# Kernel optimization log

Measured on AMD Instinct MI355X. Metric: run time of the kernel, lower is better.

The kernel has to match this reference:

```python
import jax, jax.numpy as jnp
import numpy as np
from jax import lax

DT = 0.1


def setup_inputs() -> dict:
    key = jax.random.key(0)
    k1, k2, k3, k4 = jax.random.split(key, 4)
    Bsz, L, D, N, O = 32, 2048, 256, 64, 256
    x = jax.random.normal(k1, (Bsz, L, D), dtype=jnp.float32)
    # Shift A by 3*I so Re(eig(A)) > 0 -> bilinear-discretized A_tilde is stable
    A = jax.random.uniform(k2, (N, N), dtype=jnp.float32) + 3.0 * jnp.eye(N, dtype=jnp.float32)
    B = jax.random.uniform(k3, (N, D), dtype=jnp.float32)
    C = jax.random.uniform(k4, (O, N), dtype=jnp.float32)
    return {"x": x, "A": A, "B": B, "C": C}


def _s4_forward(x, A, B, C):
    N = A.shape[0]
    I = jnp.eye(N, dtype=A.dtype)
    # Bilinear discretization (as written in the torch source)
    tmp_inv = jnp.linalg.inv(I + A * (DT / 2))
    A_tilde = tmp_inv @ (I - A * (DT / 2))          # [N, N]
    B_tilde = (tmp_inv @ B) * DT                    # [N, D]

    L = x.shape[1]

    # K[i] = C @ A_tilde^i @ B_tilde; carry M = A_tilde^i @ B_tilde
    def step(M, _):
        return A_tilde @ M, C @ M                    # emit [O, D]

    _, K = lax.scan(step, B_tilde, None, length=L)   # K: [L, O, D]

    n = 2 * L - 1  # length after torch's F.pad(x, (0,0,0,L-1))
    x_fft = jnp.fft.rfft(x, n=n, axis=1)             # [B, F, D] complex
    K_fft = jnp.fft.rfft(K, n=n, axis=0)             # [F, O, D] complex
    y_fft = jnp.einsum('bfi,foi->bfo', x_fft, K_fft)
    y = jnp.fft.irfft(y_fft, n=n, axis=1)[:, :L]     # [B, L, O]
    return y


def reference(x, A, B, C):
    return _s4_forward(x, A, B, C)
```

## Files before the change

kernel.cpp:

```cpp
#include <hip/hip_runtime.h>

#define B_SZ   32
#define LEN    2048
#define DIM    256
#define NST    64
#define OUTD   256
#define CHUNK  64
#define NCHUNK (LEN / CHUNK)
#define ROWS   (B_SZ * LEN)

#define OFF_AT   0
#define OFF_A64  4096
#define OFF_MT   8192
#define OFF_S    12288
#define OFF_INST 77824
#define OFF_U    143360
#define OFF_H    4337664
#define OFF_V    OFF_H
#define WS_FLOATS (OFF_H + ROWS * 64)

__global__ __launch_bounds__(256) void k_fused0(const float* __restrict__ A,
                                                const float* __restrict__ Bm,
                                                const float* __restrict__ x,
                                                float* __restrict__ ws) {
  __shared__ __align__(16) float sh[9088];
  const int t = threadIdx.x;

  if (blockIdx.x == 0) {
    float* Pa  = sh;
    float* Pb  = sh + 4352;
    float* rbM = sh + 8704;
    float* rbI = sh + 8832;
    float* cb  = sh + 8960;

    const int tc = t & 63;
    const int tr = t >> 6;
    float M[16], Iv[16];
    for (int i = 0; i < 16; ++i) {
      int r = 16 * tr + i;
      M[i] = 0.05f * A[r * 64 + tc] + (r == tc ? 1.0f : 0.0f);
      Iv[i] = (r == tc) ? 1.0f : 0.0f;
    }
    if (tr == 0) { rbM[tc] = M[0]; rbI[tc] = Iv[0]; }
    if (tc == 0)
      for (int i = 0; i < 16; ++i) cb[16 * tr + i] = M[i];
    __syncthreads();

#pragma unroll
    for (int k = 0; k < 64; ++k) {
      const int cur = (k & 1) * 64, nxt = ((k + 1) & 1) * 64;
      float rinv = 1.0f / rbM[cur + k];
      float rM = rbM[cur + tc] * rinv;
      float rI = rbI[cur + tc] * rinv;
#pragma unroll
      for (int i = 0; i < 16; ++i) {
        int r = 16 * tr + i;
        if (r == k) { M[i] = rM; Iv[i] = rI; }
        else {
          float f = cb[cur + r];
          M[i] = fmaf(-f, rM, M[i]);
          Iv[i] = fmaf(-f, rI, Iv[i]);
        }
      }
      if (k < 63) {
        if (tr == ((k + 1) >> 4)) {
          rbM[nxt + tc] = M[(k + 1) & 15];
          rbI[nxt + tc] = Iv[(k + 1) & 15];
        }
        if (tc == k + 1)
          for (int i = 0; i < 16; ++i) cb[nxt + 16 * tr + i] = M[i];
      }
      __syncthreads();
    }

    for (int i = 0; i < 16; ++i) {
      int r = 16 * tr + i;
      ws[OFF_AT + r * 64 + tc] = 2.0f * Iv[i] - (r == tc ? 1.0f : 0.0f);
      Pa[r * 65 + tc] = Iv[i];
    }
    __syncthreads();
    for (int i = 0; i < 16; ++i) {
      int m = 16 * tr + i;
      ws[OFF_MT + m * 64 + tc] = Pa[tc * 65 + m];
    }
    __syncthreads();

    for (int i = 0; i < 16; ++i) {
      int r = 16 * tr + i;
      Pa[r * 68 + tc] = 2.0f * Iv[i] - (r == tc ? 1.0f : 0.0f);
    }
    __syncthreads();
    float* src = Pa; float* dst = Pb;
    const int r0 = 4 * (t >> 4), c0 = 4 * (t & 15);
    for (int it = 0; it < 6; ++it) {
      float acc[4][4] = {};
      for (int k = 0; k < 64; ++k) {
        float4 bv = *(const float4*)(src + k * 68 + c0);
        for (int i = 0; i < 4; ++i) {
          float av = src[(r0 + i) * 68 + k];
          acc[i][0] = fmaf(av, bv.x, acc[i][0]);
          acc[i][1] = fmaf(av, bv.y, acc[i][1]);
          acc[i][2] = fmaf(av, bv.z, acc[i][2]);
          acc[i][3] = fmaf(av, bv.w, acc[i][3]);
        }
      }
      for (int i = 0; i < 4; ++i)
        *(float4*)(dst + (r0 + i) * 68 + c0) =
            make_float4(acc[i][0], acc[i][1], acc[i][2], acc[i][3]);
      __syncthreads();
      float* tmp = src; src = dst; dst = tmp;
    }
    for (int i = 0; i < 4; ++i) {
      int f = 4 * (t + 256 * i);
      int r = f >> 6, c = f & 63;
      *(float4*)(ws + OFF_A64 + f) = *(const float4*)(src + r * 68 + c);
    }
  } else {
    float* xsT = sh;
    float* bsT = sh + 4352;
    const int rowbase = (blockIdx.x - 1) * 64;
    const int r0 = 4 * (t >> 4), m0 = 4 * (t & 15);
    float acc[4][4] = {};
    for (int db = 0; db < 4; ++db) {
      int d0 = db * 64;
      for (int i = 0; i < 4; ++i) {
        int e = 4 * (t + 256 * i);
        int rr = e >> 6, dd = e & 63;
        float4 xv = *(const float4*)(x + (size_t)(rowbase + rr) * 256 + d0 + dd);
        xsT[(dd + 0) * 68 + rr] = xv.x;
        xsT[(dd + 1) * 68 + rr] = xv.y;
        xsT[(dd + 2) * 68 + rr] = xv.z;
        xsT[(dd + 3) * 68 + rr] = xv.w;
        float4 bv = *(const float4*)(Bm + (size_t)rr * 256 + d0 + dd);
        bsT[(dd + 0) * 68 + rr] = bv.x;
        bsT[(dd + 1) * 68 + rr] = bv.y;
        bsT[(dd + 2) * 68 + rr] = bv.z;
        bsT[(dd + 3) * 68 + rr] = bv.w;
      }
      __syncthreads();
      for (int k = 0; k < 64; ++k) {
        float4 av4 = *(const float4*)(xsT + k * 68 + r0);
        float4 bv4 = *(const float4*)(bsT + k * 68 + m0);
        float av[4] = {av4.x, av4.y, av4.z, av4.w};
        float bv[4] = {bv4.x, bv4.y, bv4.z, bv4.w};
        for (int i = 0; i < 4; ++i)
          for (int j = 0; j < 4; ++j) acc[i][j] = fmaf(av[i], bv[j], acc[i][j]);
      }
      __syncthreads();
    }
    float* v = ws + OFF_V;
    for (int i = 0; i < 4; ++i)
      *(float4*)(v + (size_t)(rowbase + r0 + i) * 64 + m0) =
          make_float4(acc[i][0], acc[i][1], acc[i][2], acc[i][3]);
  }
}

__global__ __launch_bounds__(256) void k_umm(float* __restrict__ ws) {
  __shared__ __align__(16) float vT[64 * 68];
  __shared__ __align__(16) float mts[64 * 68];
  const int t = threadIdx.x;
  const int rowbase = blockIdx.x * 64;
  const float* v = ws + OFF_V;
  for (int i = 0; i < 4; ++i) {
    int e = 4 * (t + 256 * i);
    int rr = e >> 6, mm = e & 63;
    *(float4*)(mts + rr * 68 + mm) = *(const float4*)(ws + OFF_MT + e);
    float4 vv = *(const float4*)(v + (size_t)(rowbase + rr) * 64 + mm);
    vT[(mm + 0) * 68 + rr] = vv.x;
    vT[(mm + 1) * 68 + rr] = vv.y;
    vT[(mm + 2) * 68 + rr] = vv.z;
    vT[(mm + 3) * 68 + rr] = vv.w;
  }
  __syncthreads();
  const int r0 = 4 * (t >> 4), n0 = 4 * (t & 15);
  float acc[4][4] = {};
  for (int k = 0; k < 64; ++k) {
    float4 av4 = *(const float4*)(vT + k * 68 + r0);
    float4 bv4 = *(const float4*)(mts + k * 68 + n0);
    float av[4] = {av4.x, av4.y, av4.z, av4.w};
    float bv[4] = {bv4.x, bv4.y, bv4.z, bv4.w};
    for (int i = 0; i < 4; ++i)
      for (int j = 0; j < 4; ++j) acc[i][j] = fmaf(av[i], bv[j], acc[i][j]);
  }
  float* u = ws + OFF_U;
  for (int i = 0; i < 4; ++i)
    *(float4*)(u + (size_t)(rowbase + r0 + i) * 64 + n0) =
        make_float4(0.1f * acc[i][0], 0.1f * acc[i][1], 0.1f * acc[i][2],
                    0.1f * acc[i][3]);
}

__device__ __forceinline__ void load_areg(const float* __restrict__ M, int r,
                                          int q, float areg[16]) {
  const float4* ap = (const float4*)(M + r * 64 + q * 16);
  float4 a0 = ap[0], a1 = ap[1], a2 = ap[2], a3 = ap[3];
  areg[0] = a0.x; areg[1] = a0.y; areg[2] = a0.z; areg[3] = a0.w;
  areg[4] = a1.x; areg[5] = a1.y; areg[6] = a1.z; areg[7] = a1.w;
  areg[8] = a2.x; areg[9] = a2.y; areg[10] = a2.z; areg[11] = a2.w;
  areg[12] = a3.x; areg[13] = a3.y; areg[14] = a3.z; areg[15] = a3.w;
}

__device__ __forceinline__ float matvec_step(const float areg[16],
                                             const float* __restrict__ hcur,
                                             float* __restrict__ part, int r,
                                             int q, int t) {
  float4 ha = *(const float4*)(hcur + q * 16);
  float4 hb = *(const float4*)(hcur + q * 16 + 4);
  float4 hc = *(const float4*)(hcur + q * 16 + 8);
  float4 hd = *(const float4*)(hcur + q * 16 + 12);
  float p0 = fmaf(areg[0], ha.x, fmaf(areg[4], hb.x, fmaf(areg[8], hc.x, areg[12] * hd.x)));
  float p1 = fmaf(areg[1], ha.y, fmaf(areg[5], hb.y, fmaf(areg[9], hc.y, areg[13] * hd.y)));
  float p2 = fmaf(areg[2], ha.z, fmaf(areg[6], hb.z, fmaf(areg[10], hc.z, areg[14] * hd.z)));
  float p3 = fmaf(areg[3], ha.w, fmaf(areg[7], hb.w, fmaf(areg[11], hc.w, areg[15] * hd.w)));
  part[q * 68 + r] = (p0 + p1) + (p2 + p3);
  __syncthreads();
  float s = 0.0f;
  if (t < 64) s = part[t] + part[68 + t] + part[136 + t] + part[204 + t];
  return s;
}

__global__ __launch_bounds__(256) void k_chunk(float* __restrict__ ws, int phase) {
  __shared__ __align__(16) float hcur[64];
  __shared__ __align__(16) float part[4 * 68];
  __shared__ __align__(16) float ulds[CHUNK * 64];
  const int t = threadIdx.x;
  const int c = blockIdx.x, b = blockIdx.y;
  const int r = t & 63, q = t >> 6;
  float areg[16];
  load_areg(ws + OFF_AT, r, q, areg);
  const float* u = ws + OFF_U + (size_t)(b * LEN + c * CHUNK) * 64;
  for (int i = 0; i < 4; ++i) {
    int e = 4 * (t + 256 * i);
    *(float4*)(ulds + e) = *(const float4*)(u + e);
  }
  if (t < 64)
    hcur[t] = (phase == 3) ? ws[OFF_INST + (b * NCHUNK + c) * 64 + t] : 0.0f;
  __syncthreads();
  for (int st = 0; st < CHUNK; ++st) {
    float s = matvec_step(areg, hcur, part, r, q, t);
    if (t < 64) {
      float hn = s + ulds[st * 64 + t];
      hcur[t] = hn;
      if (phase == 3)
        ws[OFF_H + (size_t)(b * LEN + c * CHUNK + st) * 64 + t] = hn;
      else if (st == CHUNK - 1)
        ws[OFF_S + (b * NCHUNK + c) * 64 + t] = hn;
    }
    __syncthreads();
  }
}

__global__ __launch_bounds__(256) void k_carry(float* __restrict__ ws) {
  __shared__ __align__(16) float hcur[64];
  __shared__ __align__(16) float part[4 * 68];
  __shared__ __align__(16) float slds[NCHUNK * 64];
  const int t = threadIdx.x;
  const int b = blockIdx.x;
  const int r = t & 63, q = t >> 6;
  float areg[16];
  load_areg(ws + OFF_A64, r, q, areg);
  for (int i = 0; i < 2; ++i) {
    int e = 4 * (t + 256 * i);
    *(float4*)(slds + e) = *(const float4*)(ws + OFF_S + b * NCHUNK * 64 + e);
  }
  if (t < 64) {
    hcur[t] = 0.0f;
    ws[OFF_INST + (b * NCHUNK) * 64 + t] = 0.0f;
  }
  __syncthreads();
  for (int c = 1; c < NCHUNK; ++c) {
    float s = matvec_step(areg, hcur, part, r, q, t);
    if (t < 64) {
      float hn = s + slds[(c - 1) * 64 + t];
      hcur[t] = hn;
      ws[OFF_INST + (b * NCHUNK + c) * 64 + t] = hn;
    }
    __syncthreads();
  }
}

__global__ __launch_bounds__(256) void k_ygemm(const float* __restrict__ Cm,
                                               const float* __restrict__ ws,
                                               float* __restrict__ y) {
  __shared__ __align__(16) float hs[64 * 68];
  __shared__ __align__(16) float cs[64 * 68];
  const int t = threadIdx.x;
  const int rowbase = blockIdx.x * 64;
  const int o0 = blockIdx.y * 64;
  const float* h = ws + OFF_H;
  for (int i = 0; i < 4; ++i) {
    int e = 4 * (t + 256 * i);
    int rr = e >> 6, nn = e & 63;
    *(float4*)(hs + rr * 68 + nn) =
        *(const float4*)(h + (size_t)rowbase * 64 + e);
    float4 cv = *(const float4*)(Cm + (size_t)(o0 + rr) * 64 + nn);
    cs[(nn + 0) * 68 + rr] = cv.x;
    cs[(nn + 1) * 68 + rr] = cv.y;
    cs[(nn + 2) * 68 + rr] = cv.z;
    cs[(nn + 3) * 68 + rr] = cv.w;
  }
  __syncthreads();
  const int tr = t >> 4, tc = t & 15;
  const int r0 = tr * 4, c0 = tc * 4;
  float acc[4][4] = {};
  for (int k = 0; k < 64; ++k) {
    float4 cv4 = *(const float4*)(cs + k * 68 + c0);
    float cv[4] = {cv4.x, cv4.y, cv4.z, cv4.w};
    for (int i = 0; i < 4; ++i) {
      float hv = hs[(r0 + i) * 68 + k];
      for (int j = 0; j < 4; ++j) acc[i][j] = fmaf(hv, cv[j], acc[i][j]);
    }
  }
  for (int i = 0; i < 4; ++i)
    *(float4*)(y + (size_t)(rowbase + r0 + i) * 256 + o0 + c0) =
        make_float4(acc[i][0], acc[i][1], acc[i][2], acc[i][3]);
}

extern "C" void kernel_launch(void* const* d_in, const int* in_sizes, int n_in,
                              void* d_out, int out_size, void* d_ws,
                              size_t ws_size, hipStream_t stream) {
  const float* x = (const float*)d_in[0];
  const float* A = (const float*)d_in[1];
  const float* Bm = (const float*)d_in[2];
  const float* Cm = (const float*)d_in[3];
  float* y = (float*)d_out;
  float* ws = (float*)d_ws;
  if (ws_size < (size_t)WS_FLOATS * sizeof(float)) return;

  hipLaunchKernelGGL(k_fused0, dim3(1 + ROWS / 64), dim3(256), 0, stream, A, Bm,
                     x, ws);
  hipLaunchKernelGGL(k_umm, dim3(ROWS / 64), dim3(256), 0, stream, ws);
  hipLaunchKernelGGL(k_chunk, dim3(NCHUNK, B_SZ), dim3(256), 0, stream, ws, 1);
  hipLaunchKernelGGL(k_carry, dim3(B_SZ), dim3(256), 0, stream, ws);
  hipLaunchKernelGGL(k_chunk, dim3(NCHUNK, B_SZ), dim3(256), 0, stream, ws, 3);
  hipLaunchKernelGGL(k_ygemm, dim3(ROWS / 64, OUTD / 64), dim3(256), 0, stream,
                     Cm, ws, y);
}
```

Before: 258.8 us.

## Fold input matrix into output projection, drop k_umm, retile GEMMs with async LDS loads

Stops transforming the x·B product by the inverse matrix in a separate k_umm pass. Instead the scan runs on the untransformed state v, and the inverse (times DT) is folded into a precomputed C' = 0.1·C·Inv used by the output GEMM. This removes one full-size GEMM pass and its global-memory round trip. The x·B and y GEMMs are retiled to 128-row tiles with 8x4 and 8x8 register blocking, XOR-swizzled LDS, double buffering and global_load_lds direct loads, which raises register pressure and lowers occupancy.

```diff
diff --git a/kernel.cpp b/kernel.cpp
--- a/kernel.cpp
+++ b/kernel.cpp
@@ -11,27 +11,61 @@
 
 #define OFF_AT   0
 #define OFF_A64  4096
-#define OFF_MT   8192
-#define OFF_S    12288
-#define OFF_INST 77824
-#define OFF_U    143360
-#define OFF_H    4337664
-#define OFF_V    OFF_H
-#define WS_FLOATS (OFF_H + ROWS * 64)
+#define OFF_CP   8192
+#define OFF_S    24576
+#define OFF_INST 90112
+#define OFF_V    155648
+#define OFF_H    OFF_V
+#define WS_FLOATS (OFF_V + (size_t)ROWS * 64)
+
+__device__ __forceinline__ void gload16(const float* gp, float* lds_base,
+                                        int lane_off_f) {
+#if __has_builtin(__builtin_amdgcn_global_load_lds)
+  (void)lane_off_f;
+  __builtin_amdgcn_global_load_lds(
+      (const __attribute__((address_space(1))) unsigned int*)gp,
+      (__attribute__((address_space(3))) unsigned int*)lds_base, 16, 0, 0);
+#else
+  float4 tmp = *(const float4*)gp;
+  *(float4*)(lds_base + lane_off_f) = tmp;
+#endif
+}
+
+__device__ __forceinline__ void mm64(float* dst, const float* a, const float* b,
+                                     int t) {
+  const int r0 = 4 * (t >> 4), c0 = 4 * (t & 15);
+  float acc[4][4] = {};
+  for (int k = 0; k < 64; ++k) {
+    float4 bv = *(const float4*)(b + k * 68 + c0);
+    for (int i = 0; i < 4; ++i) {
+      float av = a[(r0 + i) * 68 + k];
+      acc[i][0] = fmaf(av, bv.x, acc[i][0]);
+      acc[i][1] = fmaf(av, bv.y, acc[i][1]);
+      acc[i][2] = fmaf(av, bv.z, acc[i][2]);
+      acc[i][3] = fmaf(av, bv.w, acc[i][3]);
+    }
+  }
+  for (int i = 0; i < 4; ++i)
+    *(float4*)(dst + (r0 + i) * 68 + c0) =
+        make_float4(acc[i][0], acc[i][1], acc[i][2], acc[i][3]);
+  __syncthreads();
+}
 
 __global__ __launch_bounds__(256) void k_fused0(const float* __restrict__ A,
                                                 const float* __restrict__ Bm,
+                                                const float* __restrict__ Cm,
                                                 const float* __restrict__ x,
                                                 float* __restrict__ ws) {
-  __shared__ __align__(16) float sh[9088];
+  __shared__ __align__(16) float sh[13056];
   const int t = threadIdx.x;
 
   if (blockIdx.x == 0) {
-    float* Pa  = sh;
-    float* Pb  = sh + 4352;
-    float* rbM = sh + 8704;
-    float* rbI = sh + 8832;
-    float* cb  = sh + 8960;
+    float* Pa = sh;
+    float* Pb = sh + 4352;
+    float* Pc = sh + 8704;
+    float* rbM = Pc;
+    float* rbI = Pc + 128;
+    float* cb  = Pc + 256;
 
     const int tc = t & 63;
     const int tr = t >> 6;
@@ -75,118 +109,120 @@
 
     for (int i = 0; i < 16; ++i) {
       int r = 16 * tr + i;
-      ws[OFF_AT + r * 64 + tc] = 2.0f * Iv[i] - (r == tc ? 1.0f : 0.0f);
-      Pa[r * 65 + tc] = Iv[i];
-    }
-    __syncthreads();
-    for (int i = 0; i < 16; ++i) {
-      int m = 16 * tr + i;
-      ws[OFF_MT + m * 64 + tc] = Pa[tc * 65 + m];
-    }
-    __syncthreads();
-
+      float at = 2.0f * Iv[i] - (r == tc ? 1.0f : 0.0f);
+      ws[OFF_AT + r * 64 + tc] = at;
+      Pa[r * 68 + tc] = at;
+      Pc[r * 68 + tc] = Iv[i];
+    }
+    __syncthreads();
+
+    mm64(Pb, Pa, Pa, t);
+    mm64(Pa, Pb, Pb, t);
+    mm64(Pb, Pa, Pa, t);
+    mm64(Pa, Pb, Pb, t);
+    mm64(Pb, Pa, Pa, t);
+    mm64(Pa, Pb, Pb, t);
     for (int i = 0; i < 16; ++i) {
       int r = 16 * tr + i;
-      Pa[r * 68 + tc] = 2.0f * Iv[i] - (r == tc ? 1.0f : 0.0f);
-    }
-    __syncthreads();
-    float* src = Pa; float* dst = Pb;
-    const int r0 = 4 * (t >> 4), c0 = 4 * (t & 15);
-    for (int it = 0; it < 6; ++it) {
-      float acc[4][4] = {};
-      for (int k = 0; k < 64; ++k) {
-        float4 bv = *(const float4*)(src + k * 68 + c0);
-        for (int i = 0; i < 4; ++i) {
-          float av = src[(r0 + i) * 68 + k];
-          acc[i][0] = fmaf(av, bv.x, acc[i][0]);
-          acc[i][1] = fmaf(av, bv.y, acc[i][1]);
-          acc[i][2] = fmaf(av, bv.z, acc[i][2]);
-          acc[i][3] = fmaf(av, bv.w, acc[i][3]);
+      ws[OFF_A64 + r * 64 + tc] = Pa[r * 68 + tc];
+    }
+
+    {
+      const float* Crow = Cm + (size_t)t * 64;
+      float4 acc4[16];
+      for (int q = 0; q < 16; ++q) acc4[q] = make_float4(0.f, 0.f, 0.f, 0.f);
+      for (int k = 0; k < 64; k += 4) {
+        float4 c4 = *(const float4*)(Crow + k);
+        float ck[4] = {c4.x, c4.y, c4.z, c4.w};
+#pragma unroll
+        for (int kk = 0; kk < 4; ++kk) {
+          const float* mrow = Pc + (k + kk) * 68;
+          float c = ck[kk];
+#pragma unroll
+          for (int q = 0; q < 16; ++q) {
+            float4 mv = *(const float4*)(mrow + 4 * q);
+            acc4[q].x = fmaf(c, mv.x, acc4[q].x);
+            acc4[q].y = fmaf(c, mv.y, acc4[q].y);
+            acc4[q].z = fmaf(c, mv.z, acc4[q].z);
+            acc4[q].w = fmaf(c, mv.w, acc4[q].w);
+          }
         }
       }
-      for (int i = 0; i < 4; ++i)
-        *(float4*)(dst + (r0 + i) * 68 + c0) =
-            make_float4(acc[i][0], acc[i][1], acc[i][2], acc[i][3]);
+      float* cp = ws + OFF_CP + (size_t)t * 64;
+      for (int q = 0; q < 16; ++q)
+        *(float4*)(cp + 4 * q) =
+            make_float4(0.1f * acc4[q].x, 0.1f * acc4[q].y, 0.1f * acc4[q].z,
+                        0.1f * acc4[q].w);
+    }
+  } else {
+    float* xs0 = sh;
+    float* xs1 = sh + 4096;
+    float* bs0 = sh + 8192;
+    float* bs1 = sh + 10240;
+    const int w = t >> 6, lane = t & 63;
+    const int ro8 = lane >> 3, kq8 = lane & 7;
+    const int rowbase = ((int)blockIdx.x - 1) * 128;
+
+    auto stage = [&](int d0, float* xbuf, float* bbuf) {
+#pragma unroll
+      for (int c = 0; c < 4; ++c) {
+        int q = 4 * w + c;
+        const float* gp = x + (size_t)(rowbase + 8 * q + ro8) * 256 + d0 +
+                          4 * (kq8 ^ (q & 7));
+        gload16(gp, xbuf + q * 256, lane * 4);
+      }
+#pragma unroll
+      for (int c = 0; c < 2; ++c) {
+        int q = 2 * w + c;
+        const float* gp =
+            Bm + (size_t)(8 * q + ro8) * 256 + d0 + 4 * (kq8 ^ q);
+        gload16(gp, bbuf + q * 256, lane * 4);
+      }
+    };
+
+    stage(0, xs0, bs0);
+    const int g = lane >> 4, lm = lane & 15;
+    const int r0 = 32 * w + 8 * g, m0 = 4 * lm;
+    const int ka = 4 * ((4 * w + g) & 7);
+    const int kb = 4 * ((lm >> 1) & 7);
+    float acc[8][4] = {};
+    float* xc = xs0; float* xn = xs1; float* bc = bs0; float* bn = bs1;
+    __syncthreads();
+
+    for (int s = 0; s < 8; ++s) {
+      if (s < 7) stage((s + 1) * 32, xn, bn);
+      const float* xa = xc + r0 * 32;
+      const float* bb = bc + m0 * 32;
+#pragma unroll
+      for (int k0 = 0; k0 < 32; k0 += 4) {
+        float4 a4[8], b4[4];
+#pragma unroll
+        for (int i = 0; i < 8; ++i)
+          a4[i] = *(const float4*)(xa + i * 32 + (k0 ^ ka));
+#pragma unroll
+        for (int j = 0; j < 4; ++j)
+          b4[j] = *(const float4*)(bb + j * 32 + (k0 ^ kb));
+#pragma unroll
+        for (int i = 0; i < 8; ++i)
+#pragma unroll
+          for (int j = 0; j < 4; ++j) {
+            acc[i][j] = fmaf(a4[i].x, b4[j].x, acc[i][j]);
+            acc[i][j] = fmaf(a4[i].y, b4[j].y, acc[i][j]);
+            acc[i][j] = fmaf(a4[i].z, b4[j].z, acc[i][j]);
+            acc[i][j] = fmaf(a4[i].w, b4[j].w, acc[i][j]);
+          }
+      }
       __syncthreads();
-      float* tmp = src; src = dst; dst = tmp;
-    }
-    for (int i = 0; i < 4; ++i) {
-      int f = 4 * (t + 256 * i);
-      int r = f >> 6, c = f & 63;
-      *(float4*)(ws + OFF_A64 + f) = *(const float4*)(src + r * 68 + c);
-    }
-  } else {
-    float* xsT = sh;
-    float* bsT = sh + 4352;
-    const int rowbase = (blockIdx.x - 1) * 64;
-    const int r0 = 4 * (t >> 4), m0 = 4 * (t & 15);
-    float acc[4][4] = {};
-    for (int db = 0; db < 4; ++db) {
-      int d0 = db * 64;
-      for (int i = 0; i < 4; ++i) {
-        int e = 4 * (t + 256 * i);
-        int rr = e >> 6, dd = e & 63;
-        float4 xv = *(const float4*)(x + (size_t)(rowbase + rr) * 256 + d0 + dd);
-        xsT[(dd + 0) * 68 + rr] = xv.x;
-        xsT[(dd + 1) * 68 + rr] = xv.y;
-        xsT[(dd + 2) * 68 + rr] = xv.z;
-        xsT[(dd + 3) * 68 + rr] = xv.w;
-        float4 bv = *(const float4*)(Bm + (size_t)rr * 256 + d0 + dd);
-        bsT[(dd + 0) * 68 + rr] = bv.x;
-        bsT[(dd + 1) * 68 + rr] = bv.y;
-        bsT[(dd + 2) * 68 + rr] = bv.z;
-        bsT[(dd + 3) * 68 + rr] = bv.w;
-      }
-      __syncthreads();
-      for (int k = 0; k < 64; ++k) {
-        float4 av4 = *(const float4*)(xsT + k * 68 + r0);
-        float4 bv4 = *(const float4*)(bsT + k * 68 + m0);
-        float av[4] = {av4.x, av4.y, av4.z, av4.w};
-        float bv[4] = {bv4.x, bv4.y, bv4.z, bv4.w};
-        for (int i = 0; i < 4; ++i)
-          for (int j = 0; j < 4; ++j) acc[i][j] = fmaf(av[i], bv[j], acc[i][j]);
-      }
-      __syncthreads();
+      float* tp;
+      tp = xc; xc = xn; xn = tp;
+      tp = bc; bc = bn; bn = tp;
     }
     float* v = ws + OFF_V;
-    for (int i = 0; i < 4; ++i)
+#pragma unroll
+    for (int i = 0; i < 8; ++i)
       *(float4*)(v + (size_t)(rowbase + r0 + i) * 64 + m0) =
           make_float4(acc[i][0], acc[i][1], acc[i][2], acc[i][3]);
   }
-}
-
-__global__ __launch_bounds__(256) void k_umm(float* __restrict__ ws) {
-  __shared__ __align__(16) float vT[64 * 68];
-  __shared__ __align__(16) float mts[64 * 68];
-  const int t = threadIdx.x;
-  const int rowbase = blockIdx.x * 64;
-  const float* v = ws + OFF_V;
-  for (int i = 0; i < 4; ++i) {
-    int e = 4 * (t + 256 * i);
-    int rr = e >> 6, mm = e & 63;
-    *(float4*)(mts + rr * 68 + mm) = *(const float4*)(ws + OFF_MT + e);
-    float4 vv = *(const float4*)(v + (size_t)(rowbase + rr) * 64 + mm);
-    vT[(mm + 0) * 68 + rr] = vv.x;
-    vT[(mm + 1) * 68 + rr] = vv.y;
-    vT[(mm + 2) * 68 + rr] = vv.z;
-    vT[(mm + 3) * 68 + rr] = vv.w;
-  }
-  __syncthreads();
-  const int r0 = 4 * (t >> 4), n0 = 4 * (t & 15);
-  float acc[4][4] = {};
-  for (int k = 0; k < 64; ++k) {
-    float4 av4 = *(const float4*)(vT + k * 68 + r0);
-    float4 bv4 = *(const float4*)(mts + k * 68 + n0);
-    float av[4] = {av4.x, av4.y, av4.z, av4.w};
-    float bv[4] = {bv4.x, bv4.y, bv4.z, bv4.w};
-    for (int i = 0; i < 4; ++i)
-      for (int j = 0; j < 4; ++j) acc[i][j] = fmaf(av[i], bv[j], acc[i][j]);
-  }
-  float* u = ws + OFF_U;
-  for (int i = 0; i < 4; ++i)
-    *(float4*)(u + (size_t)(rowbase + r0 + i) * 64 + n0) =
-        make_float4(0.1f * acc[i][0], 0.1f * acc[i][1], 0.1f * acc[i][2],
-                    0.1f * acc[i][3]);
 }
 
 __device__ __forceinline__ void load_areg(const float* __restrict__ M, int r,
@@ -227,7 +263,7 @@
   const int r = t & 63, q = t >> 6;
   float areg[16];
   load_areg(ws + OFF_AT, r, q, areg);
-  const float* u = ws + OFF_U + (size_t)(b * LEN + c * CHUNK) * 64;
+  const float* u = ws + OFF_V + (size_t)(b * LEN + c * CHUNK) * 64;
   for (int i = 0; i < 4; ++i) {
     int e = 4 * (t + 256 * i);
     *(float4*)(ulds + e) = *(const float4*)(u + e);
@@ -278,41 +314,61 @@
   }
 }
 
-__global__ __launch_bounds__(256) void k_ygemm(const float* __restrict__ Cm,
-                                               const float* __restrict__ ws,
+__global__ __launch_bounds__(256) void k_ygemm(const float* __restrict__ ws,
                                                float* __restrict__ y) {
-  __shared__ __align__(16) float hs[64 * 68];
-  __shared__ __align__(16) float cs[64 * 68];
+  __shared__ __align__(16) float sh[16384];
+  float* hs = sh;
+  float* cs = sh + 8192;
   const int t = threadIdx.x;
-  const int rowbase = blockIdx.x * 64;
-  const int o0 = blockIdx.y * 64;
-  const float* h = ws + OFF_H;
-  for (int i = 0; i < 4; ++i) {
-    int e = 4 * (t + 256 * i);
-    int rr = e >> 6, nn = e & 63;
-    *(float4*)(hs + rr * 68 + nn) =
-        *(const float4*)(h + (size_t)rowbase * 64 + e);
-    float4 cv = *(const float4*)(Cm + (size_t)(o0 + rr) * 64 + nn);
-    cs[(nn + 0) * 68 + rr] = cv.x;
-    cs[(nn + 1) * 68 + rr] = cv.y;
-    cs[(nn + 2) * 68 + rr] = cv.z;
-    cs[(nn + 3) * 68 + rr] = cv.w;
-  }
-  __syncthreads();
-  const int tr = t >> 4, tc = t & 15;
-  const int r0 = tr * 4, c0 = tc * 4;
-  float acc[4][4] = {};
-  for (int k = 0; k < 64; ++k) {
-    float4 cv4 = *(const float4*)(cs + k * 68 + c0);
-    float cv[4] = {cv4.x, cv4.y, cv4.z, cv4.w};
-    for (int i = 0; i < 4; ++i) {
-      float hv = hs[(r0 + i) * 68 + k];
-      for (int j = 0; j < 4; ++j) acc[i][j] = fmaf(hv, cv[j], acc[i][j]);
-    }
-  }
-  for (int i = 0; i < 4; ++i)
-    *(float4*)(y + (size_t)(rowbase + r0 + i) * 256 + o0 + c0) =
-        make_float4(acc[i][0], acc[i][1], acc[i][2], acc[i][3]);
+  const int w = t >> 6, lane = t & 63;
+  const int rowbase = blockIdx.x * 128;
+  const int obase = blockIdx.y * 128;
+  const float* H = ws + OFF_H;
+  const float* CP = ws + OFF_CP;
+
+  const int ro4 = lane >> 4, kq16 = lane & 15;
+#pragma unroll
+  for (int c = 0; c < 8; ++c) {
+    int q = 8 * w + c;
+    int row = 4 * q + ro4;
+    int sd = 4 * (kq16 ^ ((row >> 3) & 7));
+    gload16(H + (size_t)(rowbase + row) * 64 + sd, hs + q * 256, lane * 4);
+    gload16(CP + (size_t)(obase + row) * 64 + sd, cs + q * 256, lane * 4);
+  }
+  __syncthreads();
+
+  const int g = lane >> 4, lm = lane & 15;
+  const int r0 = 32 * w + 8 * g, o0 = 8 * lm;
+  const int ka = 4 * ((4 * w + g) & 7);
+  const int kb = 4 * (lm & 7);
+  const float* ha = hs + r0 * 64;
+  const float* cbp = cs + o0 * 64;
+  float acc[8][8] = {};
+#pragma unroll
+  for (int k0 = 0; k0 < 64; k0 += 4) {
+    float4 a4[8], b4[8];
+#pragma unroll
+    for (int i = 0; i < 8; ++i)
+      a4[i] = *(const float4*)(ha + i * 64 + (k0 ^ ka));
+#pragma unroll
+    for (int j = 0; j < 8; ++j)
+      b4[j] = *(const float4*)(cbp + j * 64 + (k0 ^ kb));
+#pragma unroll
+    for (int i = 0; i < 8; ++i)
+#pragma unroll
+      for (int j = 0; j < 8; ++j) {
+        acc[i][j] = fmaf(a4[i].x, b4[j].x, acc[i][j]);
+        acc[i][j] = fmaf(a4[i].y, b4[j].y, acc[i][j]);
+        acc[i][j] = fmaf(a4[i].z, b4[j].z, acc[i][j]);
+        acc[i][j] = fmaf(a4[i].w, b4[j].w, acc[i][j]);
+      }
+  }
+#pragma unroll
+  for (int i = 0; i < 8; ++i) {
+    float* yp = y + (size_t)(rowbase + r0 + i) * 256 + obase + o0;
+    *(float4*)(yp) = make_float4(acc[i][0], acc[i][1], acc[i][2], acc[i][3]);
+    *(float4*)(yp + 4) = make_float4(acc[i][4], acc[i][5], acc[i][6], acc[i][7]);
+  }
 }
 
 extern "C" void kernel_launch(void* const* d_in, const int* in_sizes, int n_in,
@@ -326,12 +382,11 @@
   float* ws = (float*)d_ws;
   if (ws_size < (size_t)WS_FLOATS * sizeof(float)) return;
 
-  hipLaunchKernelGGL(k_fused0, dim3(1 + ROWS / 64), dim3(256), 0, stream, A, Bm,
-                     x, ws);
-  hipLaunchKernelGGL(k_umm, dim3(ROWS / 64), dim3(256), 0, stream, ws);
+  hipLaunchKernelGGL(k_fused0, dim3(1 + ROWS / 128), dim3(256), 0, stream, A,
+                     Bm, Cm, x, ws);
   hipLaunchKernelGGL(k_chunk, dim3(NCHUNK, B_SZ), dim3(256), 0, stream, ws, 1);
   hipLaunchKernelGGL(k_carry, dim3(B_SZ), dim3(256), 0, stream, ws);
   hipLaunchKernelGGL(k_chunk, dim3(NCHUNK, B_SZ), dim3(256), 0, stream, ws, 3);
-  hipLaunchKernelGGL(k_ygemm, dim3(ROWS / 64, OUTD / 64), dim3(256), 0, stream,
-                     Cm, ws, y);
-}
+  hipLaunchKernelGGL(k_ygemm, dim3(ROWS / 128, OUTD / 128), dim3(256), 0,
+                     stream, ws, y);
+}
```

New measurement: 260.3 us. About the same (+0.5%).
